# Kernel optimization log

Measured on AMD Instinct MI355X. Metric: run time of the kernel, lower is better.

## Reference

```python
import jax, jax.numpy as jnp
import numpy as np
import math

B, S, H = 4, 1024, 768
NH, DH = 12, 64
POS = 2 * S
INIT_STD = 0.02


def rel_shift_bnij(x, klen):
    # x: [b, n, i, j] -> Transformer-XL relative shift
    b, n, i, j = x.shape
    x = x.reshape(b, n, j, i)
    x = x[:, :, 1:, :]
    x = x.reshape(b, n, i, j - 1)
    return x[:, :, :, :klen]


def setup_inputs() -> dict:
    key = jax.random.key(0)
    ks = jax.random.split(key, 10)
    hidden = jax.random.normal(ks[0], (B, S, H), dtype=jnp.float32)
    pos_emb = jax.random.normal(ks[1], (B, POS, H), dtype=jnp.float32)
    mask = (jax.random.uniform(ks[2], (B, S, S)) < 0.1).astype(jnp.float32)
    q = INIT_STD * jax.random.normal(ks[3], (H, NH, DH), dtype=jnp.float32)
    kv = INIT_STD * jax.random.normal(ks[4], (H, NH, DH), dtype=jnp.float32)
    r = INIT_STD * jax.random.normal(ks[5], (H, NH, DH), dtype=jnp.float32)
    r_r_bias = INIT_STD * jax.random.normal(ks[6], (NH, DH), dtype=jnp.float32)
    r_w_bias = INIT_STD * jax.random.normal(ks[7], (NH, DH), dtype=jnp.float32)
    w_out = INIT_STD * jax.random.normal(ks[8], (NH * DH, H), dtype=jnp.float32)
    b_out = jnp.zeros((H,), dtype=jnp.float32)
    return {"hidden": hidden, "pos_emb": pos_emb, "mask": mask,
            "q": q, "kv": kv, "r": r,
            "r_r_bias": r_r_bias, "r_w_bias": r_w_bias,
            "w_out": w_out, "b_out": b_out}


def reference(hidden, pos_emb, mask, q, kv, r, r_r_bias, r_w_bias, w_out, b_out):
    b, s, dim = hidden.shape
    d_head = q.shape[-1]
    q_head_h = jnp.einsum('bih,hnd->bind', hidden, q)
    kv_head_h = jnp.einsum('bih,hnd->bind', hidden, kv)
    k_head_r = jnp.einsum('bih,hnd->bind', pos_emb, r)
    # content and position score terms
    ac = jnp.einsum('bind,bjnd->bnij', q_head_h + r_w_bias, kv_head_h)
    bd = jnp.einsum('bind,bjnd->bnij', q_head_h + r_r_bias, k_head_r)
    bd = rel_shift_bnij(bd, klen=ac.shape[3])
    scores = (ac + bd) / math.sqrt(d_head)
    scores = scores + mask[:, None, :, :] * (-65500.0)
    alpha = jax.nn.softmax(scores, axis=-1)  # dropout is identity in eval
    res = jnp.einsum('bhmn,bnhd->bmhd', alpha, kv_head_h).reshape(b, s, dim)
    res = res @ w_out + b_out
    res = hidden + res  # graph_residual=True
    return jax.nn.gelu(res, approximate=False)
```

## Files before the change

### kernel.cpp

```cpp
#include <hip/hip_runtime.h>

typedef unsigned short u16;
typedef unsigned int u32;
typedef unsigned long long u64;
typedef __attribute__((ext_vector_type(8))) short bf8v;
typedef __attribute__((ext_vector_type(4))) float f32x4;
typedef __attribute__((ext_vector_type(4))) u32 u32x4;

#define S_   1024
#define POS_ 2048

__device__ __forceinline__ float b2f(u16 h){
  union { float f; unsigned u; } x; x.u = ((unsigned)h) << 16; return x.f;
}
__device__ __forceinline__ u16 f2b(float f){
  union { float f; unsigned u; } x; x.f = f;
  unsigned u = x.u;
  return (u16)((u + 0x7fffu + ((u >> 16) & 1u)) >> 16);
}
__device__ __forceinline__ u16 f2bt(float f){
  union { float f; unsigned u; } x; x.f = f;
  return (u16)(x.u >> 16);
}

#define GLDS16(g, l) __builtin_amdgcn_global_load_lds( \
    (const __attribute__((address_space(1))) unsigned int*)(g), \
    (__attribute__((address_space(3))) unsigned int*)(l), 16, 0, 0)

__global__ __launch_bounds__(256) void transpose_w(const float* __restrict__ q, const float* __restrict__ kv,
                                                   const float* __restrict__ r, const float* __restrict__ wo,
                                                   u16* __restrict__ wqkv, u16* __restrict__ wout){
  __shared__ u16 t[32][33];
  const float* src; u16* dst;
  int z = blockIdx.z;
  if (z == 0){ src = q;  dst = wqkv; }
  else if (z == 1){ src = kv; dst = wqkv + 768*768; }
  else if (z == 2){ src = r;  dst = wqkv + 2*768*768; }
  else { src = wo; dst = wout; }
  int gx = blockIdx.x*32, gy = blockIdx.y*32;
  int tx = threadIdx.x, ty = threadIdx.y;
  #pragma unroll
  for (int k = 0; k < 4; ++k)
    t[ty + 8*k][tx] = f2b(src[(gy + ty + 8*k)*768 + gx + tx]);
  __syncthreads();
  #pragma unroll
  for (int k = 0; k < 4; ++k)
    dst[(gx + ty + 8*k)*768 + gy + tx] = t[tx][ty + 8*k];
}

__global__ __launch_bounds__(256) void maskprep(const float* __restrict__ mask, u64* __restrict__ mb){
  int widx = blockIdx.x*4 + (threadIdx.x >> 6);
  int lane = threadIdx.x & 63;
  int kt = widx & 15, ig = widx >> 4;
  float m = mask[(size_t)ig*1024 + kt*64 + lane];
  u64 bits = __ballot(m != 0.0f);
  if (lane == 0) mb[(size_t)((ig >> 10)*16 + kt)*1024 + (ig & 1023)] = bits;
}

__global__ __launch_bounds__(256) void conv_bf16(const float* __restrict__ a, const float* __restrict__ b,
                                                 u16* __restrict__ da, u16* __restrict__ db){
  size_t i = ((size_t)blockIdx.x*256 + threadIdx.x)*8;
  const float* s; u16* d;
  if (i < 3145728){ s = a + i; d = da + i; }
  else { s = b + (i - 3145728); d = db + (i - 3145728); }
  f32x4 x0 = *(const f32x4*)s, x1 = *(const f32x4*)(s + 4);
  bf8v t;
  #pragma unroll
  for (int j = 0; j < 4; ++j){ t[j] = f2b(x0[j]); t[4+j] = f2b(x1[j]); }
  *(bf8v*)d = t;
}

template<int MODE>
__device__ __forceinline__ void gemm_core(const void* Av, int lda, const u16* Bt,
                                          void* Cv, int ldc,
                                          const float* resid, const float* bias,
                                          int bm, int bn,
                                          u16 (*As)[32], u16 (*Bs)[32]){
  int tid = threadIdx.x;
  int lane = tid & 63, rg = tid >> 6;
  int quad = lane >> 4, l15 = lane & 15;
  int wm = rg >> 1, wn = rg & 1;
  int poff = (quad ^ ((l15 >> 1) & 3)) * 8;
  f32x4 acc[4][4];
  #pragma unroll
  for (int i = 0; i < 4; ++i)
    #pragma unroll
    for (int j = 0; j < 4; ++j)
      acc[i][j] = (f32x4){0.f,0.f,0.f,0.f};

  for (int kt = 0; kt < 24; ++kt){
    int k0 = kt*32;
    if (kt) __syncthreads();
    #pragma unroll
    for (int t = 0; t < 2; ++t){
      int m = (rg*2 + t)*16 + (lane >> 2);
      int g = ((lane & 3) ^ ((m >> 1) & 3)) * 8;
      GLDS16(&Bt[(size_t)(bn*128 + m)*768 + k0 + g], &Bs[m][(lane & 3)*8]);
    }
    if (MODE & 2){
      #pragma unroll
      for (int t = 0; t < 2; ++t){
        int m = (rg*2 + t)*16 + (lane >> 2);
        int g = ((lane & 3) ^ ((m >> 1) & 3)) * 8;
        GLDS16(&((const u16*)Av)[(size_t)(bm*128 + m)*lda + k0 + g], &As[m][(lane & 3)*8]);
      }
    } else {
      #pragma unroll
      for (int e = 0; e < 2; ++e){
        int v = tid + 256*e;
        int m = v >> 2, c = v & 3;
        const u32* ap = (const u32*)Av + (size_t)(bm*128 + m)*lda + k0 + c*8;
        u32x4 a0 = *(const u32x4*)ap;
        u32x4 a1 = *(const u32x4*)(ap + 4);
        u32x4 pk;
        pk[0] = (a0[0] >> 16) | (a0[1] & 0xFFFF0000u);
        pk[1] = (a0[2] >> 16) | (a0[3] & 0xFFFF0000u);
        pk[2] = (a1[0] >> 16) | (a1[1] & 0xFFFF0000u);
        pk[3] = (a1[2] >> 16) | (a1[3] & 0xFFFF0000u);
        *(u32x4*)&As[m][(c ^ ((m >> 1) & 3))*8] = pk;
      }
    }
    __syncthreads();
    bf8v af[4], bf[4];
    #pragma unroll
    for (int mt = 0; mt < 4; ++mt) af[mt] = *(const bf8v*)&As[wm*64 + mt*16 + l15][poff];
    #pragma unroll
    for (int nt = 0; nt < 4; ++nt) bf[nt] = *(const bf8v*)&Bs[wn*64 + nt*16 + l15][poff];
    #pragma unroll
    for (int mt = 0; mt < 4; ++mt)
      #pragma unroll
      for (int nt = 0; nt < 4; ++nt)
        acc[mt][nt] = __builtin_amdgcn_mfma_f32_16x16x32_bf16(af[mt], bf[nt], acc[mt][nt], 0, 0, 0);
  }

  #pragma unroll
  for (int mt = 0; mt < 4; ++mt){
    #pragma unroll
    for (int nt = 0; nt < 4; ++nt){
      #pragma unroll
      for (int reg = 0; reg < 4; ++reg){
        int grow = bm*128 + wm*64 + mt*16 + quad*4 + reg;
        int gcol = bn*128 + wn*64 + nt*16 + l15;
        float v = acc[mt][nt][reg];
        if (MODE & 1){
          v += bias[gcol] + resid[(size_t)grow*ldc + gcol];
          v = 0.5f * v * (1.0f + erff(v * 0.70710678118654752f));
          ((float*)Cv)[(size_t)grow*ldc + gcol] = v;
        } else {
          ((u16*)Cv)[(size_t)grow*ldc + gcol] = f2b(v);
        }
      }
    }
  }
}

__global__ __launch_bounds__(256) void gemm_proj(const void* __restrict__ A1, const void* __restrict__ A2,
                                                 const u16* __restrict__ wqkv,
                                                 u16* __restrict__ qkvh, u16* __restrict__ krh, int amode){
  __shared__ u16 As[128][32];
  __shared__ u16 Bs[128][32];
  int t = blockIdx.x;
  if (t < 384){
    if (amode) gemm_core<2>(A1, 768, wqkv, qkvh, 1536, nullptr, nullptr, t & 31, t >> 5, As, Bs);
    else       gemm_core<0>(A1, 768, wqkv, qkvh, 1536, nullptr, nullptr, t & 31, t >> 5, As, Bs);
  } else {
    t -= 384;
    if (amode) gemm_core<2>(A2, 768, wqkv + 2*768*768, krh, 768, nullptr, nullptr, t & 63, t >> 6, As, Bs);
    else       gemm_core<0>(A2, 768, wqkv + 2*768*768, krh, 768, nullptr, nullptr, t & 63, t >> 6, As, Bs);
  }
}

__global__ __launch_bounds__(256) void gemm_out(const u16* __restrict__ ctx, const u16* __restrict__ wout,
                                                float* __restrict__ out,
                                                const float* __restrict__ resid, const float* __restrict__ bias){
  __shared__ u16 As[128][32];
  __shared__ u16 Bs[128][32];
  gemm_core<3>(ctx, 768, wout, out, 768, resid, bias, blockIdx.x, blockIdx.y, As, Bs);
}

__global__ __launch_bounds__(256) void attn(const u16* __restrict__ qkvh,
                                            const u16* __restrict__ krh,
                                            const u64* __restrict__ mb,
                                            const float* __restrict__ rrb,
                                            const float* __restrict__ rwb,
                                            u16* __restrict__ ctx){
  __shared__ u16 kvL[64][72];
  __shared__ u16 krL[96][72];
  __shared__ u16 pL[32][72];
  __shared__ u64 mL[32];
  __shared__ float lpart[4][32];

  int tid = threadIdx.x;
  int lane = tid & 63, w = tid >> 6;
  int quad = lane >> 4, l15 = lane & 15;

  int fid = blockIdx.x;
  int xcd = fid & 7, loc = fid >> 3;
  int pair = xcd*6 + (loc >> 5);
  int i0 = (loc & 31) * 32;
  int b = pair / 12, n = pair % 12;

  const u16* kvbase = qkvh + (size_t)b*S_*1536 + 768 + n*64;
  const u16* krbase = krh + (size_t)b*POS_*768 + n*64;

  {
    int r = tid >> 3, d0 = (tid & 7)*8;
    bf8v qv = *(const bf8v*)&qkvh[(size_t)(b*S_ + i0 + r)*1536 + n*64 + d0];
    f32x4 w0 = *(const f32x4*)&rwb[n*64 + d0];
    f32x4 w1 = *(const f32x4*)&rwb[n*64 + d0 + 4];
    f32x4 r0 = *(const f32x4*)&rrb[n*64 + d0];
    f32x4 r1 = *(const f32x4*)&rrb[n*64 + d0 + 4];
    bf8v qw, qr;
    #pragma unroll
    for (int j = 0; j < 4; ++j){
      float qf0 = b2f((u16)qv[j]), qf1 = b2f((u16)qv[4+j]);
      qw[j]   = f2b((qf0 + w0[j])*0.125f);
      qw[4+j] = f2b((qf1 + w1[j])*0.125f);
      qr[j]   = f2b((qf0 + r0[j])*0.125f);
      qr[4+j] = f2b((qf1 + r1[j])*0.125f);
    }
    *(bf8v*)&krL[r][d0]      = qw;
    *(bf8v*)&krL[32 + r][d0] = qr;
  }
  __syncthreads();
  bf8v qwf[2][2], qrf[2][2];
  #pragma unroll
  for (int rgi = 0; rgi < 2; ++rgi)
    #pragma unroll
    for (int c = 0; c < 2; ++c){
      qwf[rgi][c] = *(const bf8v*)&krL[rgi*16 + l15][c*32 + quad*8];
      qrf[rgi][c] = *(const bf8v*)&krL[32 + rgi*16 + l15][c*32 + quad*8];
    }

  f32x4 ctxa[2];
  float l_acc[2][4];
  #pragma unroll
  for (int i = 0; i < 2; ++i){
    ctxa[i] = (f32x4){0.f,0.f,0.f,0.f};
    #pragma unroll
    for (int j = 0; j < 4; ++j) l_acc[i][j] = 0.f;
  }

  int key = w*16 + l15;
  for (int kt = 0; kt < 16; ++kt){
    int k0 = kt*64;
    int j0 = k0 + S_ - i0 - 31;
    __syncthreads();
    #pragma unroll
    for (int e = 0; e < 2; ++e){
      int v = tid + 256*e;
      int kk = v >> 3, d0 = (v & 7)*8;
      int col = (d0 + 8*((kk >> 3) & 7)) & 63;
      *(bf8v*)&kvL[kk][col] = *(const bf8v*)&kvbase[(size_t)(k0 + kk)*1536 + d0];
    }
    #pragma unroll
    for (int e = 0; e < 3; ++e){
      int v = tid + 256*e;
      int jj = v >> 3, d0 = (v & 7)*8;
      int jg = j0 + jj;
      bf8v val;
      if (jg < POS_) val = *(const bf8v*)&krbase[(size_t)jg*768 + d0];
      else           val = (bf8v){0,0,0,0,0,0,0,0};
      *(bf8v*)&krL[jj][d0] = val;
    }
    if (tid < 32) mL[tid] = mb[(size_t)(b*16 + kt)*1024 + i0 + tid];
    __syncthreads();

    #pragma unroll
    for (int rgi = 0; rgi < 2; ++rgi){
      f32x4 ac = (f32x4){0.f,0.f,0.f,0.f};
      #pragma unroll
      for (int c = 0; c < 2; ++c){
        bf8v bk = *(const bf8v*)&kvL[key][(c*32 + quad*8 + 8*((key >> 3) & 7)) & 63];
        ac = __builtin_amdgcn_mfma_f32_16x16x32_bf16(qwf[rgi][c], bk, ac, 0, 0, 0);
      }
      int base = (w - rgi)*16 + 16;
      f32x4 bd0 = (f32x4){0.f,0.f,0.f,0.f}, bd1 = (f32x4){0.f,0.f,0.f,0.f};
      #pragma unroll
      for (int c = 0; c < 2; ++c){
        bf8v bk0 = *(const bf8v*)&krL[base + l15][c*32 + quad*8];
        bf8v bk1 = *(const bf8v*)&krL[base + 16 + l15][c*32 + quad*8];
        bd0 = __builtin_amdgcn_mfma_f32_16x16x32_bf16(qrf[rgi][c], bk0, bd0, 0, 0, 0);
        bd1 = __builtin_amdgcn_mfma_f32_16x16x32_bf16(qrf[rgi][c], bk1, bd1, 0, 0, 0);
      }
      #pragma unroll
      for (int reg = 0; reg < 4; ++reg){
        int rloc = rgi*16 + quad*4 + reg;
        u64 wbits = mL[rloc];
        int sj = l15 + 15 - (quad*4 + reg);
        int srcl = (sj & 15) | (lane & 48);
        float v0 = __shfl(bd0[reg], srcl);
        float v1 = __shfl(bd1[reg], srcl);
        float s = ac[reg] + ((sj < 16) ? v0 : v1);
        if ((wbits >> key) & 1ull) s -= 65500.0f;
        float p = __expf(s);
        l_acc[rgi][reg] += p;
        pL[rloc][key] = f2bt(p);
      }
    }
    __syncthreads();

    bf8v bv[2];
    #pragma unroll
    for (int c = 0; c < 2; ++c){
      int col = (key + 8*(4*c + quad)) & 63;
      #pragma unroll
      for (int j = 0; j < 8; ++j)
        bv[c][j] = (short)kvL[c*32 + quad*8 + j][col];
    }
    #pragma unroll
    for (int rgi = 0; rgi < 2; ++rgi)
      #pragma unroll
      for (int c = 0; c < 2; ++c){
        bf8v pa = *(const bf8v*)&pL[rgi*16 + l15][c*32 + quad*8];
        ctxa[rgi] = __builtin_amdgcn_mfma_f32_16x16x32_bf16(pa, bv[c], ctxa[rgi], 0, 0, 0);
      }
  }

  #pragma unroll
  for (int rgi = 0; rgi < 2; ++rgi)
    #pragma unroll
    for (int reg = 0; reg < 4; ++reg){
      float v = l_acc[rgi][reg];
      #pragma unroll
      for (int off = 1; off < 16; off <<= 1) v += __shfl_xor(v, off);
      l_acc[rgi][reg] = v;
    }
  if (l15 == 0){
    #pragma unroll
    for (int rgi = 0; rgi < 2; ++rgi)
      #pragma unroll
      for (int reg = 0; reg < 4; ++reg)
        lpart[w][rgi*16 + quad*4 + reg] = l_acc[rgi][reg];
  }
  __syncthreads();
  #pragma unroll
  for (int rgi = 0; rgi < 2; ++rgi)
    #pragma unroll
    for (int reg = 0; reg < 4; ++reg){
      int rloc = rgi*16 + quad*4 + reg;
      float lt = lpart[0][rloc] + lpart[1][rloc] + lpart[2][rloc] + lpart[3][rloc];
      ctx[(size_t)(b*S_ + i0 + rloc)*768 + n*64 + w*16 + l15] = f2b(ctxa[rgi][reg] / lt);
    }
}

extern "C" void kernel_launch(void* const* d_in, const int* in_sizes, int n_in,
                              void* d_out, int out_size, void* d_ws, size_t ws_size,
                              hipStream_t stream){
  (void)in_sizes; (void)n_in; (void)out_size;
  const float* hidden = (const float*)d_in[0];
  const float* pos    = (const float*)d_in[1];
  const float* maskp  = (const float*)d_in[2];
  const float* q      = (const float*)d_in[3];
  const float* kv     = (const float*)d_in[4];
  const float* r      = (const float*)d_in[5];
  const float* rrb    = (const float*)d_in[6];
  const float* rwb    = (const float*)d_in[7];
  const float* wo     = (const float*)d_in[8];
  const float* bo     = (const float*)d_in[9];
  float* out = (float*)d_out;

  u16* qkvh = (u16*)d_ws;
  u16* krh  = qkvh + (size_t)4096*1536;
  u16* wout = krh  + (size_t)8192*768;
  u16* wqkv = wout + 768*768;
  bool big = ws_size >= 49283072ull;
  u16 *hb = nullptr, *pb = nullptr, *ctx;
  u64* mbp;
  if (big){
    hb  = wqkv + (size_t)3*768*768;
    pb  = hb + (size_t)4096*768;
    ctx = hb;
    mbp = (u64*)(pb + (size_t)8192*768);
  } else {
    ctx = wqkv;
    mbp = (u64*)(wqkv + (size_t)4096*768);
  }

  transpose_w<<<dim3(24,24,4), dim3(32,8), 0, stream>>>(q, kv, r, wo, wqkv, wout);
  maskprep<<<dim3(16384), 256, 0, stream>>>(maskp, mbp);
  if (big){
    conv_bf16<<<dim3(4608), 256, 0, stream>>>(hidden, pos, hb, pb);
    gemm_proj<<<dim3(768), 256, 0, stream>>>(hb, pb, wqkv, qkvh, krh, 2);
  } else {
    gemm_proj<<<dim3(768), 256, 0, stream>>>(hidden, pos, wqkv, qkvh, krh, 0);
  }
  attn<<<dim3(1536), 256, 0, stream>>>(qkvh, krh, mbp, rrb, rwb, ctx);
  gemm_out<<<dim3(32,6), 256, 0, stream>>>(ctx, wout, out, hidden, bo);
}
```

Before: 268.0 us.

## Merge prep kernels, use async LDS loads in attention, retile output GEMM

Result: faster. 232.4 us (-13.3%).

```diff
diff --git a/kernel.cpp b/kernel.cpp
--- a/kernel.cpp
+++ b/kernel.cpp
@@ -27,53 +27,55 @@
     (const __attribute__((address_space(1))) unsigned int*)(g), \
     (__attribute__((address_space(3))) unsigned int*)(l), 16, 0, 0)
 
-__global__ __launch_bounds__(256) void transpose_w(const float* __restrict__ q, const float* __restrict__ kv,
-                                                   const float* __restrict__ r, const float* __restrict__ wo,
-                                                   u16* __restrict__ wqkv, u16* __restrict__ wout){
-  __shared__ u16 t[32][33];
-  const float* src; u16* dst;
-  int z = blockIdx.z;
-  if (z == 0){ src = q;  dst = wqkv; }
-  else if (z == 1){ src = kv; dst = wqkv + 768*768; }
-  else if (z == 2){ src = r;  dst = wqkv + 2*768*768; }
-  else { src = wo; dst = wout; }
-  int gx = blockIdx.x*32, gy = blockIdx.y*32;
-  int tx = threadIdx.x, ty = threadIdx.y;
-  #pragma unroll
-  for (int k = 0; k < 4; ++k)
-    t[ty + 8*k][tx] = f2b(src[(gy + ty + 8*k)*768 + gx + tx]);
-  __syncthreads();
-  #pragma unroll
-  for (int k = 0; k < 4; ++k)
-    dst[(gx + ty + 8*k)*768 + gy + tx] = t[tx][ty + 8*k];
-}
-
-__global__ __launch_bounds__(256) void maskprep(const float* __restrict__ mask, u64* __restrict__ mb){
-  int widx = blockIdx.x*4 + (threadIdx.x >> 6);
-  int lane = threadIdx.x & 63;
-  int kt = widx & 15, ig = widx >> 4;
-  float m = mask[(size_t)ig*1024 + kt*64 + lane];
-  u64 bits = __ballot(m != 0.0f);
-  if (lane == 0) mb[(size_t)((ig >> 10)*16 + kt)*1024 + (ig & 1023)] = bits;
-}
-
-__global__ __launch_bounds__(256) void conv_bf16(const float* __restrict__ a, const float* __restrict__ b,
-                                                 u16* __restrict__ da, u16* __restrict__ db){
-  size_t i = ((size_t)blockIdx.x*256 + threadIdx.x)*8;
-  const float* s; u16* d;
-  if (i < 3145728){ s = a + i; d = da + i; }
-  else { s = b + (i - 3145728); d = db + (i - 3145728); }
-  f32x4 x0 = *(const f32x4*)s, x1 = *(const f32x4*)(s + 4);
-  bf8v t;
-  #pragma unroll
-  for (int j = 0; j < 4; ++j){ t[j] = f2b(x0[j]); t[4+j] = f2b(x1[j]); }
-  *(bf8v*)d = t;
+__global__ __launch_bounds__(256) void prep(const float* __restrict__ q, const float* __restrict__ kv,
+                                            const float* __restrict__ r, const float* __restrict__ wo,
+                                            u16* __restrict__ wqkv, u16* __restrict__ wout,
+                                            const float* __restrict__ mask, u64* __restrict__ mb,
+                                            u16* __restrict__ zp,
+                                            const float* __restrict__ hidden, const float* __restrict__ pos,
+                                            u16* __restrict__ hb, u16* __restrict__ pb){
+  int blk = blockIdx.x, tid = threadIdx.x;
+  if (blk < 2304){
+    __shared__ u16 t[32][33];
+    int z = blk / 576, rem = blk % 576;
+    const float* src; u16* dst;
+    if (z == 0){ src = q;  dst = wqkv; }
+    else if (z == 1){ src = kv; dst = wqkv + 768*768; }
+    else if (z == 2){ src = r;  dst = wqkv + 2*768*768; }
+    else { src = wo; dst = wout; }
+    int gx = (rem % 24)*32, gy = (rem / 24)*32;
+    int tx = tid & 31, ty = tid >> 5;
+    #pragma unroll
+    for (int k = 0; k < 4; ++k)
+      t[ty + 8*k][tx] = f2b(src[(gy + ty + 8*k)*768 + gx + tx]);
+    __syncthreads();
+    #pragma unroll
+    for (int k = 0; k < 4; ++k)
+      dst[(gx + ty + 8*k)*768 + gy + tx] = t[tx][ty + 8*k];
+  } else if (blk < 18688){
+    int widx = (blk - 2304)*4 + (tid >> 6);
+    int lane = tid & 63;
+    int kt = widx & 15, ig = widx >> 4;
+    float m = mask[(size_t)ig*1024 + kt*64 + lane];
+    u64 bits = __ballot(m != 0.0f);
+    if (lane == 0) mb[(size_t)((ig >> 10)*16 + kt)*1024 + (ig & 1023)] = bits;
+    if (blk == 2304 && tid < 8) zp[tid] = 0;
+  } else {
+    size_t i = ((size_t)(blk - 18688)*256 + tid)*8;
+    const float* s; u16* d;
+    if (i < 3145728){ s = hidden + i; d = hb + i; }
+    else { s = pos + (i - 3145728); d = pb + (i - 3145728); }
+    f32x4 x0 = *(const f32x4*)s, x1 = *(const f32x4*)(s + 4);
+    bf8v t;
+    #pragma unroll
+    for (int j = 0; j < 4; ++j){ t[j] = f2b(x0[j]); t[4+j] = f2b(x1[j]); }
+    *(bf8v*)d = t;
+  }
 }
 
 template<int MODE>
 __device__ __forceinline__ void gemm_core(const void* Av, int lda, const u16* Bt,
-                                          void* Cv, int ldc,
-                                          const float* resid, const float* bias,
+                                          u16* Cv, int ldc,
                                           int bm, int bn,
                                           u16 (*As)[32], u16 (*Bs)[32]){
   int tid = threadIdx.x;
@@ -134,24 +136,15 @@
   }
 
   #pragma unroll
-  for (int mt = 0; mt < 4; ++mt){
-    #pragma unroll
-    for (int nt = 0; nt < 4; ++nt){
+  for (int mt = 0; mt < 4; ++mt)
+    #pragma unroll
+    for (int nt = 0; nt < 4; ++nt)
       #pragma unroll
       for (int reg = 0; reg < 4; ++reg){
         int grow = bm*128 + wm*64 + mt*16 + quad*4 + reg;
         int gcol = bn*128 + wn*64 + nt*16 + l15;
-        float v = acc[mt][nt][reg];
-        if (MODE & 1){
-          v += bias[gcol] + resid[(size_t)grow*ldc + gcol];
-          v = 0.5f * v * (1.0f + erff(v * 0.70710678118654752f));
-          ((float*)Cv)[(size_t)grow*ldc + gcol] = v;
-        } else {
-          ((u16*)Cv)[(size_t)grow*ldc + gcol] = f2b(v);
-        }
-      }
-    }
-  }
+        Cv[(size_t)grow*ldc + gcol] = f2b(acc[mt][nt][reg]);
+      }
 }
 
 __global__ __launch_bounds__(256) void gemm_proj(const void* __restrict__ A1, const void* __restrict__ A2,
@@ -161,21 +154,63 @@
   __shared__ u16 Bs[128][32];
   int t = blockIdx.x;
   if (t < 384){
-    if (amode) gemm_core<2>(A1, 768, wqkv, qkvh, 1536, nullptr, nullptr, t & 31, t >> 5, As, Bs);
-    else       gemm_core<0>(A1, 768, wqkv, qkvh, 1536, nullptr, nullptr, t & 31, t >> 5, As, Bs);
+    if (amode) gemm_core<2>(A1, 768, wqkv, qkvh, 1536, t & 31, t >> 5, As, Bs);
+    else       gemm_core<0>(A1, 768, wqkv, qkvh, 1536, t & 31, t >> 5, As, Bs);
   } else {
     t -= 384;
-    if (amode) gemm_core<2>(A2, 768, wqkv + 2*768*768, krh, 768, nullptr, nullptr, t & 63, t >> 6, As, Bs);
-    else       gemm_core<0>(A2, 768, wqkv + 2*768*768, krh, 768, nullptr, nullptr, t & 63, t >> 6, As, Bs);
+    if (amode) gemm_core<2>(A2, 768, wqkv + 2*768*768, krh, 768, t & 63, t >> 6, As, Bs);
+    else       gemm_core<0>(A2, 768, wqkv + 2*768*768, krh, 768, t & 63, t >> 6, As, Bs);
   }
 }
 
 __global__ __launch_bounds__(256) void gemm_out(const u16* __restrict__ ctx, const u16* __restrict__ wout,
                                                 float* __restrict__ out,
                                                 const float* __restrict__ resid, const float* __restrict__ bias){
-  __shared__ u16 As[128][32];
-  __shared__ u16 Bs[128][32];
-  gemm_core<3>(ctx, 768, wout, out, 768, resid, bias, blockIdx.x, blockIdx.y, As, Bs);
+  __shared__ u16 As[64][32];
+  __shared__ u16 Bs[64][32];
+  int tid = threadIdx.x;
+  int lane = tid & 63, rg = tid >> 6;
+  int quad = lane >> 4, l15 = lane & 15;
+  int wm = rg >> 1, wn = rg & 1;
+  int bm = blockIdx.x, bn = blockIdx.y;
+  f32x4 acc[2][2];
+  #pragma unroll
+  for (int i = 0; i < 2; ++i)
+    #pragma unroll
+    for (int j = 0; j < 2; ++j)
+      acc[i][j] = (f32x4){0.f,0.f,0.f,0.f};
+
+  int m = tid >> 2, s = (tid & 3)*8;
+  for (int kt = 0; kt < 24; ++kt){
+    int k0 = kt*32;
+    if (kt) __syncthreads();
+    GLDS16(&ctx[(size_t)(bm*64 + m)*768 + k0 + s], &As[m][s]);
+    GLDS16(&wout[(size_t)(bn*64 + m)*768 + k0 + s], &Bs[m][s]);
+    __syncthreads();
+    bf8v af[2], bf[2];
+    #pragma unroll
+    for (int mt = 0; mt < 2; ++mt) af[mt] = *(const bf8v*)&As[wm*32 + mt*16 + l15][quad*8];
+    #pragma unroll
+    for (int nt = 0; nt < 2; ++nt) bf[nt] = *(const bf8v*)&Bs[wn*32 + nt*16 + l15][quad*8];
+    #pragma unroll
+    for (int mt = 0; mt < 2; ++mt)
+      #pragma unroll
+      for (int nt = 0; nt < 2; ++nt)
+        acc[mt][nt] = __builtin_amdgcn_mfma_f32_16x16x32_bf16(af[mt], bf[nt], acc[mt][nt], 0, 0, 0);
+  }
+
+  #pragma unroll
+  for (int mt = 0; mt < 2; ++mt)
+    #pragma unroll
+    for (int nt = 0; nt < 2; ++nt)
+      #pragma unroll
+      for (int reg = 0; reg < 4; ++reg){
+        int grow = bm*64 + wm*32 + mt*16 + quad*4 + reg;
+        int gcol = bn*64 + wn*32 + nt*16 + l15;
+        float v = acc[mt][nt][reg] + bias[gcol] + resid[(size_t)grow*768 + gcol];
+        v = 0.5f * v * (1.0f + erff(v * 0.70710678118654752f));
+        out[(size_t)grow*768 + gcol] = v;
+      }
 }
 
 __global__ __launch_bounds__(256) void attn(const u16* __restrict__ qkvh,
@@ -183,9 +218,11 @@
                                             const u64* __restrict__ mb,
                                             const float* __restrict__ rrb,
                                             const float* __restrict__ rwb,
+                                            const u16* __restrict__ zp,
                                             u16* __restrict__ ctx){
-  __shared__ u16 kvL[64][72];
-  __shared__ u16 krL[96][72];
+  __shared__ u16 kvL[64][64];
+  __shared__ u16 krL[96][64];
+  __shared__ u16 qL[2][32][72];
   __shared__ u16 pL[32][72];
   __shared__ u64 mL[32];
   __shared__ float lpart[4][32];
@@ -219,8 +256,8 @@
       qr[j]   = f2b((qf0 + r0[j])*0.125f);
       qr[4+j] = f2b((qf1 + r1[j])*0.125f);
     }
-    *(bf8v*)&krL[r][d0]      = qw;
-    *(bf8v*)&krL[32 + r][d0] = qr;
+    *(bf8v*)&qL[0][r][d0] = qw;
+    *(bf8v*)&qL[1][r][d0] = qr;
   }
   __syncthreads();
   bf8v qwf[2][2], qrf[2][2];
@@ -228,8 +265,8 @@
   for (int rgi = 0; rgi < 2; ++rgi)
     #pragma unroll
     for (int c = 0; c < 2; ++c){
-      qwf[rgi][c] = *(const bf8v*)&krL[rgi*16 + l15][c*32 + quad*8];
-      qrf[rgi][c] = *(const bf8v*)&krL[32 + rgi*16 + l15][c*32 + quad*8];
+      qwf[rgi][c] = *(const bf8v*)&qL[0][rgi*16 + l15][c*32 + quad*8];
+      qrf[rgi][c] = *(const bf8v*)&qL[1][rgi*16 + l15][c*32 + quad*8];
     }
 
   f32x4 ctxa[2];
@@ -242,6 +279,7 @@
   }
 
   int key = w*16 + l15;
+  int pvcol = (((key >> 3) + 2*quad) & 7)*8 + (key & 7);
   for (int kt = 0; kt < 16; ++kt){
     int k0 = kt*64;
     int j0 = k0 + S_ - i0 - 31;
@@ -249,19 +287,18 @@
     #pragma unroll
     for (int e = 0; e < 2; ++e){
       int v = tid + 256*e;
-      int kk = v >> 3, d0 = (v & 7)*8;
-      int col = (d0 + 8*((kk >> 3) & 7)) & 63;
-      *(bf8v*)&kvL[kk][col] = *(const bf8v*)&kvbase[(size_t)(k0 + kk)*1536 + d0];
+      int k = v >> 3, s = v & 7;
+      int g = (s - 2*(k >> 3)) & 7;
+      GLDS16(&kvbase[(size_t)(k0 + k)*1536 + g*8], &kvL[k][s*8]);
     }
     #pragma unroll
     for (int e = 0; e < 3; ++e){
       int v = tid + 256*e;
-      int jj = v >> 3, d0 = (v & 7)*8;
+      int jj = v >> 3, s = v & 7;
+      int g = (s - 3*(jj >> 3)) & 7;
       int jg = j0 + jj;
-      bf8v val;
-      if (jg < POS_) val = *(const bf8v*)&krbase[(size_t)jg*768 + d0];
-      else           val = (bf8v){0,0,0,0,0,0,0,0};
-      *(bf8v*)&krL[jj][d0] = val;
+      const u16* src = (jg < POS_) ? &krbase[(size_t)jg*768 + g*8] : zp;
+      GLDS16(src, &krL[jj][s*8]);
     }
     if (tid < 32) mL[tid] = mb[(size_t)(b*16 + kt)*1024 + i0 + tid];
     __syncthreads();
@@ -271,15 +308,19 @@
       f32x4 ac = (f32x4){0.f,0.f,0.f,0.f};
       #pragma unroll
       for (int c = 0; c < 2; ++c){
-        bf8v bk = *(const bf8v*)&kvL[key][(c*32 + quad*8 + 8*((key >> 3) & 7)) & 63];
+        int p = (c*4 + quad + 2*(key >> 3)) & 7;
+        bf8v bk = *(const bf8v*)&kvL[key][p*8];
         ac = __builtin_amdgcn_mfma_f32_16x16x32_bf16(qwf[rgi][c], bk, ac, 0, 0, 0);
       }
       int base = (w - rgi)*16 + 16;
+      int row0 = base + l15, row1 = base + 16 + l15;
       f32x4 bd0 = (f32x4){0.f,0.f,0.f,0.f}, bd1 = (f32x4){0.f,0.f,0.f,0.f};
       #pragma unroll
       for (int c = 0; c < 2; ++c){
-        bf8v bk0 = *(const bf8v*)&krL[base + l15][c*32 + quad*8];
-        bf8v bk1 = *(const bf8v*)&krL[base + 16 + l15][c*32 + quad*8];
+        int p0 = (c*4 + quad + 3*(row0 >> 3)) & 7;
+        int p1 = (c*4 + quad + 3*(row1 >> 3)) & 7;
+        bf8v bk0 = *(const bf8v*)&krL[row0][p0*8];
+        bf8v bk1 = *(const bf8v*)&krL[row1][p1*8];
         bd0 = __builtin_amdgcn_mfma_f32_16x16x32_bf16(qrf[rgi][c], bk0, bd0, 0, 0, 0);
         bd1 = __builtin_amdgcn_mfma_f32_16x16x32_bf16(qrf[rgi][c], bk1, bd1, 0, 0, 0);
       }
@@ -291,9 +332,9 @@
         int srcl = (sj & 15) | (lane & 48);
         float v0 = __shfl(bd0[reg], srcl);
         float v1 = __shfl(bd1[reg], srcl);
-        float s = ac[reg] + ((sj < 16) ? v0 : v1);
-        if ((wbits >> key) & 1ull) s -= 65500.0f;
-        float p = __expf(s);
+        float sc = ac[reg] + ((sj < 16) ? v0 : v1);
+        if ((wbits >> key) & 1ull) sc -= 65500.0f;
+        float p = __expf(sc);
         l_acc[rgi][reg] += p;
         pL[rloc][key] = f2bt(p);
       }
@@ -302,12 +343,10 @@
 
     bf8v bv[2];
     #pragma unroll
-    for (int c = 0; c < 2; ++c){
-      int col = (key + 8*(4*c + quad)) & 63;
+    for (int c = 0; c < 2; ++c)
       #pragma unroll
       for (int j = 0; j < 8; ++j)
-        bv[c][j] = (short)kvL[c*32 + quad*8 + j][col];
-    }
+        bv[c][j] = (short)kvL[c*32 + quad*8 + j][pvcol];
     #pragma unroll
     for (int rgi = 0; rgi < 2; ++rgi)
       #pragma unroll
@@ -364,7 +403,7 @@
   u16* krh  = qkvh + (size_t)4096*1536;
   u16* wout = krh  + (size_t)8192*768;
   u16* wqkv = wout + 768*768;
-  bool big = ws_size >= 49283072ull;
+  bool big = ws_size >= 49283104ull;
   u16 *hb = nullptr, *pb = nullptr, *ctx;
   u64* mbp;
   if (big){
@@ -376,15 +415,12 @@
     ctx = wqkv;
     mbp = (u64*)(wqkv + (size_t)4096*768);
   }
-
-  transpose_w<<<dim3(24,24,4), dim3(32,8), 0, stream>>>(q, kv, r, wo, wqkv, wout);
-  maskprep<<<dim3(16384), 256, 0, stream>>>(maskp, mbp);
-  if (big){
-    conv_bf16<<<dim3(4608), 256, 0, stream>>>(hidden, pos, hb, pb);
-    gemm_proj<<<dim3(768), 256, 0, stream>>>(hb, pb, wqkv, qkvh, krh, 2);
-  } else {
-    gemm_proj<<<dim3(768), 256, 0, stream>>>(hidden, pos, wqkv, qkvh, krh, 0);
-  }
-  attn<<<dim3(1536), 256, 0, stream>>>(qkvh, krh, mbp, rrb, rwb, ctx);
-  gemm_out<<<dim3(32,6), 256, 0, stream>>>(ctx, wout, out, hidden, bo);
-}
+  u16* zp = (u16*)(mbp + 65536);
+
+  prep<<<dim3(big ? 23296 : 18688), 256, 0, stream>>>(q, kv, r, wo, wqkv, wout,
+                                                      maskp, mbp, zp, hidden, pos, hb, pb);
+  if (big) gemm_proj<<<dim3(768), 256, 0, stream>>>(hb, pb, wqkv, qkvh, krh, 2);
+  else     gemm_proj<<<dim3(768), 256, 0, stream>>>(hidden, pos, wqkv, qkvh, krh, 0);
+  attn<<<dim3(1536), 256, 0, stream>>>(qkvh, krh, mbp, rrb, rwb, zp, ctx);
+  gemm_out<<<dim3(64,12), 256, 0, stream>>>(ctx, wout, out, hidden, bo);
+}
```
